# Kernel tuning notes

Measured on AMD Instinct MI355X. Metric: run time of the kernel, lower is better.

## Reference

```python
import jax, jax.numpy as jnp
import numpy as np

T, B, F = 512, 256, 256
H1, H2, OUT = 128, 64, 5


def _gru_layer(x, w_ih, w_hh, b_ih, b_hh):
    """PyTorch-convention GRU over time-major x [T, B, F_in] -> [T, B, H].
    Gate order in weights: r, z, n. n = tanh(Wn x + bn_i + r * (Un h + bn_h))."""
    H = w_hh.shape[1]
    # Precompute input projections for all timesteps: [T, B, 3H]
    xp = jnp.einsum('tbf,gf->tbg', x, w_ih) + b_ih

    def step(h, xp_t):
        hp = h @ w_hh.T + b_hh  # [B, 3H]
        xr, xz, xn = jnp.split(xp_t, 3, axis=-1)
        hr, hz, hn = jnp.split(hp, 3, axis=-1)
        r = jax.nn.sigmoid(xr + hr)
        z = jax.nn.sigmoid(xz + hz)
        n = jnp.tanh(xn + r * hn)
        h_new = (1.0 - z) * n + z * h
        return h_new, h_new

    h0 = jnp.zeros((x.shape[1], H), dtype=x.dtype)
    _, ys = jax.lax.scan(step, h0, xp)
    return ys  # [T, B, H]


def setup_inputs() -> dict:
    key = jax.random.key(0)
    ks = jax.random.split(key, 12)
    s1 = 1.0 / np.sqrt(H1)
    s2 = 1.0 / np.sqrt(H2)
    return {
        'x': jax.random.normal(ks[0], (T, B, F), dtype=jnp.float32),
        'w_ih1': jax.random.uniform(ks[1], (3 * H1, F), jnp.float32, -s1, s1),
        'w_hh1': jax.random.uniform(ks[2], (3 * H1, H1), jnp.float32, -s1, s1),
        'b_ih1': jax.random.uniform(ks[3], (3 * H1,), jnp.float32, -s1, s1),
        'b_hh1': jax.random.uniform(ks[4], (3 * H1,), jnp.float32, -s1, s1),
        'w_ih2': jax.random.uniform(ks[5], (3 * H2, H1), jnp.float32, -s2, s2),
        'w_hh2': jax.random.uniform(ks[6], (3 * H2, H2), jnp.float32, -s2, s2),
        'b_ih2': jax.random.uniform(ks[7], (3 * H2,), jnp.float32, -s2, s2),
        'b_hh2': jax.random.uniform(ks[8], (3 * H2,), jnp.float32, -s2, s2),
        'lin_w': jax.random.uniform(ks[9], (OUT, H2), jnp.float32, -s2, s2),
        'lin_b': jax.random.uniform(ks[10], (OUT,), jnp.float32, -s2, s2),
    }


def reference(x, w_ih1, w_hh1, b_ih1, b_hh1, w_ih2, w_hh2, b_ih2, b_hh2, lin_w, lin_b):
    h1 = _gru_layer(x, w_ih1, w_hh1, b_ih1, b_hh1)   # [T, B, 128]
    h2 = _gru_layer(h1, w_ih2, w_hh2, b_ih2, b_hh2)  # [T, B, 64]
    # Faithful to the original: x[:, -1, :] selects the last BATCH element
    # across all timesteps (time-major layout), giving [T, 64].
    last = h2[:, -1, :]
    return last @ lin_w.T + lin_b  # [T, 5]
```

## Files before the change

### kernel.cpp

```cpp
#include <hip/hip_runtime.h>
#include <hip/hip_bf16.h>

#define T_STEPS 512
#define BATCH   256
#define FDIM    256
#define H1      128
#define H2      64
#define OUT_N   5
#define CHUNK   8
#define NCHUNK  (T_STEPS / CHUNK)
#define LOG2E   1.4426950408889634f

#if __has_builtin(__builtin_amdgcn_exp2f)
#define EXP2F(x) __builtin_amdgcn_exp2f(x)
#else
#define EXP2F(x) exp2f(x)
#endif
#if __has_builtin(__builtin_amdgcn_rcpf)
#define RCPF(x) __builtin_amdgcn_rcpf(x)
#else
#define RCPF(x) (1.0f / (x))
#endif

template<int CTRL>
__device__ __forceinline__ float dpp_add(float v) {
    int s = __builtin_amdgcn_update_dpp(0, __float_as_int(v), CTRL, 0xF, 0xF, true);
    return v + __int_as_float(s);
}
__device__ __forceinline__ float sig_scaled(float a) {
    return RCPF(1.0f + EXP2F(a));
}
__device__ __forceinline__ float tanh_scaled(float a) {
    return fmaf(-2.0f, RCPF(EXP2F(a) + 1.0f), 1.0f);
}

__global__ __launch_bounds__(256) void xp1_kernel(
    const float* __restrict__ x,
    const float* __restrict__ w_ih1,
    const float* __restrict__ b_ih1,
    const float* __restrict__ b_hh1,
    float* __restrict__ xp)
{
    __shared__ float xrow[FDIM];
    const int t = blockIdx.x;
    const float* xr = x + (size_t)t * BATCH * FDIM + (size_t)(BATCH - 1) * FDIM;
    if (threadIdx.x < FDIM / 4) {
        ((float4*)xrow)[threadIdx.x] = ((const float4*)xr)[threadIdx.x];
    }
    __syncthreads();
    const int q = threadIdx.x >> 2;
    const int s = threadIdx.x & 3;
    #pragma unroll
    for (int pass = 0; pass < 6; ++pass) {
        const int g = pass * 64 + q;
        const float* w = w_ih1 + (size_t)g * FDIM + (s << 2);
        float acc = 0.0f;
        #pragma unroll
        for (int c = 0; c < 16; ++c) {
            float4 wv = *(const float4*)(w + 16 * c);
            const float* xv = xrow + (s << 2) + 16 * c;
            acc = fmaf(wv.x, xv[0], acc);
            acc = fmaf(wv.y, xv[1], acc);
            acc = fmaf(wv.z, xv[2], acc);
            acc = fmaf(wv.w, xv[3], acc);
        }
        acc = dpp_add<0xB1>(acc);
        acc = dpp_add<0x4E>(acc);
        if (s == 0) {
            const bool isN = (g >= 2 * H1);
            const float badd  = isN ? 0.0f : b_hh1[g];
            const float scale = isN ? (2.0f * LOG2E) : (-LOG2E);
            xp[t * (3 * H1) + g] = scale * (acc + b_ih1[g] + badd);
        }
    }
}

__global__ __launch_bounds__(512) void gru_pipe_kernel(
    const float* __restrict__ xp,
    const float* __restrict__ w_hh1, const float* __restrict__ b_hh1,
    const float* __restrict__ w_ih2, const float* __restrict__ b_ih2,
    const float* __restrict__ w_hh2, const float* __restrict__ b_hh2,
    float* __restrict__ g_h1, unsigned int* __restrict__ flags,
    float* __restrict__ h2_all)
{
    __shared__ float h1d[2][H1];
    __shared__ float h1chunk[CHUNK * H1];
    __shared__ float h2d[2][H2];
    const int tid = threadIdx.x;
    const float sRZ = -LOG2E, sN = 2.0f * LOG2E;

    if (blockIdx.x == 0) {
        const int g  = tid >> 3;
        const int s  = tid & 7;
        const int hi = (tid >> 2) & 1;
        const int r0 = 2 * g;

        float wr0[16], wz0[16], wn0[16], wr1[16], wz1[16], wn1[16];
        {
            const float* br0 = w_hh1 + (size_t)(         r0) * H1;
            const float* bz0 = w_hh1 + (size_t)(H1     + r0) * H1;
            const float* bn0 = w_hh1 + (size_t)(2 * H1 + r0) * H1;
            #pragma unroll
            for (int c = 0; c < 4; c++) {
                const int kk = (s << 2) + 32 * c;
                float4 v0 = *(const float4*)(br0 + kk);
                float4 v1 = *(const float4*)(bz0 + kk);
                float4 v2 = *(const float4*)(bn0 + kk);
                float4 v3 = *(const float4*)(br0 + H1 + kk);
                float4 v4 = *(const float4*)(bz0 + H1 + kk);
                float4 v5 = *(const float4*)(bn0 + H1 + kk);
                wr0[4*c+0]=sRZ*v0.x; wr0[4*c+1]=sRZ*v0.y; wr0[4*c+2]=sRZ*v0.z; wr0[4*c+3]=sRZ*v0.w;
                wz0[4*c+0]=sRZ*v1.x; wz0[4*c+1]=sRZ*v1.y; wz0[4*c+2]=sRZ*v1.z; wz0[4*c+3]=sRZ*v1.w;
                wn0[4*c+0]=sN *v2.x; wn0[4*c+1]=sN *v2.y; wn0[4*c+2]=sN *v2.z; wn0[4*c+3]=sN *v2.w;
                wr1[4*c+0]=sRZ*v3.x; wr1[4*c+1]=sRZ*v3.y; wr1[4*c+2]=sRZ*v3.z; wr1[4*c+3]=sRZ*v3.w;
                wz1[4*c+0]=sRZ*v4.x; wz1[4*c+1]=sRZ*v4.y; wz1[4*c+2]=sRZ*v4.z; wz1[4*c+3]=sRZ*v4.w;
                wn1[4*c+0]=sN *v5.x; wn1[4*c+1]=sN *v5.y; wn1[4*c+2]=sN *v5.z; wn1[4*c+3]=sN *v5.w;
            }
        }
        const float bn_a = sN * b_hh1[2 * H1 + r0];
        const float bn_b = sN * b_hh1[2 * H1 + r0 + 1];
        const float bh1n_s = hi ? bn_b : bn_a;

        if (tid < H1) { h1d[0][tid] = 0.0f; h1d[1][tid] = 0.0f; }
        float h1prev = 0.0f;
        float cxr, cxz, cxn;
        {
            float2 a2 = *(const float2*)(xp + r0);
            float2 b2 = *(const float2*)(xp + H1 + r0);
            float2 c2 = *(const float2*)(xp + 2 * H1 + r0);
            cxr = hi ? a2.y : a2.x; cxz = hi ? b2.y : b2.x; cxn = hi ? c2.y : c2.x;
        }
        __syncthreads();

        #pragma unroll 2
        for (int k = 0; k < T_STEPS; ++k) {
            const float* RP = h1d[(k + 1) & 1];
            float*       WP = h1d[k & 1];
            const float* hp = RP + (s << 2);
            float ar0=0.f, az0=0.f, an0=0.f, ar1=0.f, az1=0.f, an1=0.f;
            #pragma unroll
            for (int c = 0; c < 4; c++) {
                float4 h4 = *(const float4*)(hp + 32 * c);
                ar0=fmaf(wr0[4*c+0],h4.x,ar0); az0=fmaf(wz0[4*c+0],h4.x,az0); an0=fmaf(wn0[4*c+0],h4.x,an0);
                ar1=fmaf(wr1[4*c+0],h4.x,ar1); az1=fmaf(wz1[4*c+0],h4.x,az1); an1=fmaf(wn1[4*c+0],h4.x,an1);
                ar0=fmaf(wr0[4*c+1],h4.y,ar0); az0=fmaf(wz0[4*c+1],h4.y,az0); an0=fmaf(wn0[4*c+1],h4.y,an0);
                ar1=fmaf(wr1[4*c+1],h4.y,ar1); az1=fmaf(wz1[4*c+1],h4.y,az1); an1=fmaf(wn1[4*c+1],h4.y,an1);
                ar0=fmaf(wr0[4*c+2],h4.z,ar0); az0=fmaf(wz0[4*c+2],h4.z,az0); an0=fmaf(wn0[4*c+2],h4.z,an0);
                ar1=fmaf(wr1[4*c+2],h4.z,ar1); az1=fmaf(wz1[4*c+2],h4.z,az1); an1=fmaf(wn1[4*c+2],h4.z,an1);
                ar0=fmaf(wr0[4*c+3],h4.w,ar0); az0=fmaf(wz0[4*c+3],h4.w,az0); an0=fmaf(wn0[4*c+3],h4.w,an0);
                ar1=fmaf(wr1[4*c+3],h4.w,ar1); az1=fmaf(wz1[4*c+3],h4.w,az1); an1=fmaf(wn1[4*c+3],h4.w,an1);
            }
            float2 a2, b2, c2;
            {
                const int kn = (k < T_STEPS - 1) ? (k + 1) : (T_STEPS - 1);
                const float* nx = xp + (size_t)kn * (3 * H1);
                a2 = *(const float2*)(nx + r0);
                b2 = *(const float2*)(nx + H1 + r0);
                c2 = *(const float2*)(nx + 2 * H1 + r0);
            }
            ar0=dpp_add<0xB1>(ar0); ar0=dpp_add<0x4E>(ar0); ar0=dpp_add<0x141>(ar0);
            az0=dpp_add<0xB1>(az0); az0=dpp_add<0x4E>(az0); az0=dpp_add<0x141>(az0);
            an0=dpp_add<0xB1>(an0); an0=dpp_add<0x4E>(an0); an0=dpp_add<0x141>(an0);
            ar1=dpp_add<0xB1>(ar1); ar1=dpp_add<0x4E>(ar1); ar1=dpp_add<0x141>(ar1);
            az1=dpp_add<0xB1>(az1); az1=dpp_add<0x4E>(az1); az1=dpp_add<0x141>(az1);
            an1=dpp_add<0xB1>(an1); an1=dpp_add<0x4E>(an1); an1=dpp_add<0x141>(an1);
            const float ar = hi ? ar1 : ar0;
            const float az = hi ? az1 : az0;
            const float an = hi ? an1 : an0;
            const float r1g = sig_scaled(cxr + ar);
            const float z1g = sig_scaled(cxz + az);
            const float n1g = tanh_scaled(fmaf(r1g, an + bh1n_s, cxn));
            const float h1new = fmaf(z1g, h1prev - n1g, n1g);
            h1prev = h1new;
            if ((tid & 3) == 0) {
                WP[r0 + hi] = h1new;
                __hip_atomic_store((unsigned int*)g_h1 + (size_t)k * H1 + r0 + hi,
                                   __float_as_uint(h1new),
                                   __ATOMIC_RELAXED, __HIP_MEMORY_SCOPE_AGENT);
            }
            cxr = hi ? a2.y : a2.x; cxz = hi ? b2.y : b2.x; cxn = hi ? c2.y : c2.x;
            __syncthreads();
            if (((k & (CHUNK - 1)) == CHUNK - 1) && tid == 0) {
                __hip_atomic_store(&flags[k >> 3], 1u,
                                   __ATOMIC_RELEASE, __HIP_MEMORY_SCOPE_AGENT);
            }
        }
    } else {
        const int j2 = tid >> 3, s2 = tid & 7;
        float w2r[24], w2z[24], w2n[24];
        {
            const float* ir  = w_ih2 + (size_t)(         j2) * H1;
            const float* iz  = w_ih2 + (size_t)(H2     + j2) * H1;
            const float* inn = w_ih2 + (size_t)(2 * H2 + j2) * H1;
            #pragma unroll
            for (int c = 0; c < 4; c++) {
                const int kk = (s2 << 2) + 32 * c;
                float4 vr = *(const float4*)(ir  + kk);
                float4 vz = *(const float4*)(iz  + kk);
                float4 vn = *(const float4*)(inn + kk);
                w2r[4*c+0]=sRZ*vr.x; w2r[4*c+1]=sRZ*vr.y; w2r[4*c+2]=sRZ*vr.z; w2r[4*c+3]=sRZ*vr.w;
                w2z[4*c+0]=sRZ*vz.x; w2z[4*c+1]=sRZ*vz.y; w2z[4*c+2]=sRZ*vz.z; w2z[4*c+3]=sRZ*vz.w;
                w2n[4*c+0]=sN *vn.x; w2n[4*c+1]=sN *vn.y; w2n[4*c+2]=sN *vn.z; w2n[4*c+3]=sN *vn.w;
            }
            const float* hr = w_hh2 + (size_t)(         j2) * H2;
            const float* hz = w_hh2 + (size_t)(H2     + j2) * H2;
            const float* hn = w_hh2 + (size_t)(2 * H2 + j2) * H2;
            #pragma unroll
            for (int c = 0; c < 2; c++) {
                const int kk = (s2 << 2) + 32 * c;
                const int o = 4 * (c + 4);
                float4 vr = *(const float4*)(hr + kk);
                float4 vz = *(const float4*)(hz + kk);
                float4 vn = *(const float4*)(hn + kk);
                w2r[o+0]=sRZ*vr.x; w2r[o+1]=sRZ*vr.y; w2r[o+2]=sRZ*vr.z; w2r[o+3]=sRZ*vr.w;
                w2z[o+0]=sRZ*vz.x; w2z[o+1]=sRZ*vz.y; w2z[o+2]=sRZ*vz.z; w2z[o+3]=sRZ*vz.w;
                w2n[o+0]=sN *vn.x; w2n[o+1]=sN *vn.y; w2n[o+2]=sN *vn.z; w2n[o+3]=sN *vn.w;
            }
        }
        const float b2r_s  = sRZ * (b_ih2[j2]      + b_hh2[j2]);
        const float b2z_s  = sRZ * (b_ih2[H2 + j2] + b_hh2[H2 + j2]);
        const float b2xn_s = sN  *  b_ih2[2 * H2 + j2];
        const float b2hn_s = sN  *  b_hh2[2 * H2 + j2];
        float h2prev = 0.0f;
        if (tid < H2) { h2d[0][tid] = 0.0f; h2d[1][tid] = 0.0f; }
        __syncthreads();

        #pragma unroll 1
        for (int c = 0; c < NCHUNK; ++c) {
            while (__hip_atomic_load(&flags[c], __ATOMIC_ACQUIRE,
                                     __HIP_MEMORY_SCOPE_AGENT) != 1u) {
                __builtin_amdgcn_s_sleep(8);
            }
            unsigned long long v = __hip_atomic_load(
                (const unsigned long long*)g_h1 + (size_t)c * 512 + tid,
                __ATOMIC_RELAXED, __HIP_MEMORY_SCOPE_AGENT);
            ((unsigned long long*)h1chunk)[tid] = v;
            __syncthreads();

            #pragma unroll
            for (int i = 0; i < CHUNK; ++i) {
                const int t = c * CHUNK + i;
                const float* g1p = h1chunk + i * H1 + (s2 << 2);
                const float* g2p = h2d[(i + 1) & 1] + (s2 << 2);
                float a2r = 0.f, a2z = 0.f, axn = 0.f, ahn = 0.f;
                #pragma unroll
                for (int cc = 0; cc < 4; cc++) {
                    float4 g4 = *(const float4*)(g1p + 32 * cc);
                    a2r=fmaf(w2r[4*cc+0],g4.x,a2r); a2z=fmaf(w2z[4*cc+0],g4.x,a2z); axn=fmaf(w2n[4*cc+0],g4.x,axn);
                    a2r=fmaf(w2r[4*cc+1],g4.y,a2r); a2z=fmaf(w2z[4*cc+1],g4.y,a2z); axn=fmaf(w2n[4*cc+1],g4.y,axn);
                    a2r=fmaf(w2r[4*cc+2],g4.z,a2r); a2z=fmaf(w2z[4*cc+2],g4.z,a2z); axn=fmaf(w2n[4*cc+2],g4.z,axn);
                    a2r=fmaf(w2r[4*cc+3],g4.w,a2r); a2z=fmaf(w2z[4*cc+3],g4.w,a2z); axn=fmaf(w2n[4*cc+3],g4.w,axn);
                }
                #pragma unroll
                for (int cc = 4; cc < 6; cc++) {
                    float4 g4 = *(const float4*)(g2p + 32 * (cc - 4));
                    a2r=fmaf(w2r[4*cc+0],g4.x,a2r); a2z=fmaf(w2z[4*cc+0],g4.x,a2z); ahn=fmaf(w2n[4*cc+0],g4.x,ahn);
                    a2r=fmaf(w2r[4*cc+1],g4.y,a2r); a2z=fmaf(w2z[4*cc+1],g4.y,a2z); ahn=fmaf(w2n[4*cc+1],g4.y,ahn);
                    a2r=fmaf(w2r[4*cc+2],g4.z,a2r); a2z=fmaf(w2z[4*cc+2],g4.z,a2z); ahn=fmaf(w2n[4*cc+2],g4.z,ahn);
                    a2r=fmaf(w2r[4*cc+3],g4.w,a2r); a2z=fmaf(w2z[4*cc+3],g4.w,a2z); ahn=fmaf(w2n[4*cc+3],g4.w,ahn);
                }
                a2r=dpp_add<0xB1>(a2r); a2r=dpp_add<0x4E>(a2r); a2r=dpp_add<0x141>(a2r);
                a2z=dpp_add<0xB1>(a2z); a2z=dpp_add<0x4E>(a2z); a2z=dpp_add<0x141>(a2z);
                axn=dpp_add<0xB1>(axn); axn=dpp_add<0x4E>(axn); axn=dpp_add<0x141>(axn);
                ahn=dpp_add<0xB1>(ahn); ahn=dpp_add<0x4E>(ahn); ahn=dpp_add<0x141>(ahn);
                const float r2 = sig_scaled(a2r + b2r_s);
                const float z2 = sig_scaled(a2z + b2z_s);
                const float n2 = tanh_scaled(fmaf(r2, ahn + b2hn_s, axn + b2xn_s));
                const float h2new = fmaf(z2, h2prev - n2, n2);
                h2prev = h2new;
                if (s2 == 0) {
                    h2d[i & 1][j2] = h2new;
                    h2_all[(size_t)t * H2 + j2] = h2new;
                }
                __syncthreads();
            }
        }
    }
}

__global__ __launch_bounds__(256) void head_kernel(
    const float* __restrict__ h2_all,
    const float* __restrict__ lin_w,
    const float* __restrict__ lin_b,
    float* __restrict__ out)
{
    const int t = blockIdx.x * blockDim.x + threadIdx.x;
    if (t >= T_STEPS) return;
    const float* h = h2_all + t * H2;
    #pragma unroll
    for (int o = 0; o < OUT_N; o++) {
        float acc = lin_b[o];
        const float* w = lin_w + o * H2;
        #pragma unroll
        for (int j = 0; j < H2; j += 4) {
            float4 wv = *(const float4*)(w + j);
            float4 hv = *(const float4*)(h + j);
            acc = fmaf(wv.x, hv.x, acc);
            acc = fmaf(wv.y, hv.y, acc);
            acc = fmaf(wv.z, hv.z, acc);
            acc = fmaf(wv.w, hv.w, acc);
        }
        out[t * OUT_N + o] = acc;
    }
}

extern "C" void kernel_launch(void* const* d_in, const int* in_sizes, int n_in,
                              void* d_out, int out_size, void* d_ws, size_t ws_size,
                              hipStream_t stream) {
    const float* x     = (const float*)d_in[0];
    const float* w_ih1 = (const float*)d_in[1];
    const float* w_hh1 = (const float*)d_in[2];
    const float* b_ih1 = (const float*)d_in[3];
    const float* b_hh1 = (const float*)d_in[4];
    const float* w_ih2 = (const float*)d_in[5];
    const float* w_hh2 = (const float*)d_in[6];
    const float* b_ih2 = (const float*)d_in[7];
    const float* b_hh2 = (const float*)d_in[8];
    const float* lin_w = (const float*)d_in[9];
    const float* lin_b = (const float*)d_in[10];
    float* out = (float*)d_out;

    float* xp        = (float*)d_ws;
    float* h2_all    = xp + T_STEPS * 3 * H1;
    float* g_h1      = h2_all + T_STEPS * H2;
    unsigned int* fl = (unsigned int*)(g_h1 + T_STEPS * H1);

    hipMemsetAsync(fl, 0, NCHUNK * sizeof(unsigned int), stream);
    xp1_kernel<<<T_STEPS, 256, 0, stream>>>(x, w_ih1, b_ih1, b_hh1, xp);
    gru_pipe_kernel<<<2, 512, 0, stream>>>(xp, w_hh1, b_hh1,
                                           w_ih2, b_ih2, w_hh2, b_hh2,
                                           g_h1, fl, h2_all);
    head_kernel<<<(T_STEPS + 255) / 256, 256, 0, stream>>>(h2_all, lin_w, lin_b, out);
}
```

Baseline: 586.3 us.

## Use lightweight LDS-only barriers and chunk-unroll the layer-1 recurrence loop

Replaces __syncthreads with a custom barrier that waits only on LDS counters (lgkmcnt), so the per-step barrier no longer waits for outstanding global stores or loads such as the atomic h1 publish and the xp prefetch. Global memory counters are drained only once per chunk, just before the release flag is set. The layer-1 loop is restructured into chunk and inner-step loops with the inner loop fully unrolled, and the consumer's spin-sleep is shortened. The risk is ordering correctness: the memory model is being hand-managed, and the flag publish now depends on the explicit vmcnt wait.

```diff
diff --git a/kernel.cpp b/kernel.cpp
--- a/kernel.cpp
+++ b/kernel.cpp
@@ -21,6 +21,17 @@
 #else
 #define RCPF(x) (1.0f / (x))
 #endif
+
+#define BAR() do {                                              \
+    asm volatile("s_waitcnt lgkmcnt(0)" ::: "memory");          \
+    __builtin_amdgcn_s_barrier();                               \
+    __builtin_amdgcn_sched_barrier(0);                          \
+} while (0)
+#define VBAR() do {                                             \
+    asm volatile("s_waitcnt vmcnt(0) lgkmcnt(0)" ::: "memory"); \
+    __builtin_amdgcn_s_barrier();                               \
+    __builtin_amdgcn_sched_barrier(0);                          \
+} while (0)
 
 template<int CTRL>
 __device__ __forceinline__ float dpp_add(float v) {
@@ -130,59 +141,67 @@
             float2 c2 = *(const float2*)(xp + 2 * H1 + r0);
             cxr = hi ? a2.y : a2.x; cxz = hi ? b2.y : b2.x; cxn = hi ? c2.y : c2.x;
         }
-        __syncthreads();
-
-        #pragma unroll 2
-        for (int k = 0; k < T_STEPS; ++k) {
-            const float* RP = h1d[(k + 1) & 1];
-            float*       WP = h1d[k & 1];
-            const float* hp = RP + (s << 2);
-            float ar0=0.f, az0=0.f, an0=0.f, ar1=0.f, az1=0.f, an1=0.f;
-            #pragma unroll
-            for (int c = 0; c < 4; c++) {
-                float4 h4 = *(const float4*)(hp + 32 * c);
-                ar0=fmaf(wr0[4*c+0],h4.x,ar0); az0=fmaf(wz0[4*c+0],h4.x,az0); an0=fmaf(wn0[4*c+0],h4.x,an0);
-                ar1=fmaf(wr1[4*c+0],h4.x,ar1); az1=fmaf(wz1[4*c+0],h4.x,az1); an1=fmaf(wn1[4*c+0],h4.x,an1);
-                ar0=fmaf(wr0[4*c+1],h4.y,ar0); az0=fmaf(wz0[4*c+1],h4.y,az0); an0=fmaf(wn0[4*c+1],h4.y,an0);
-                ar1=fmaf(wr1[4*c+1],h4.y,ar1); az1=fmaf(wz1[4*c+1],h4.y,az1); an1=fmaf(wn1[4*c+1],h4.y,an1);
-                ar0=fmaf(wr0[4*c+2],h4.z,ar0); az0=fmaf(wz0[4*c+2],h4.z,az0); an0=fmaf(wn0[4*c+2],h4.z,an0);
-                ar1=fmaf(wr1[4*c+2],h4.z,ar1); az1=fmaf(wz1[4*c+2],h4.z,az1); an1=fmaf(wn1[4*c+2],h4.z,an1);
-                ar0=fmaf(wr0[4*c+3],h4.w,ar0); az0=fmaf(wz0[4*c+3],h4.w,az0); an0=fmaf(wn0[4*c+3],h4.w,an0);
-                ar1=fmaf(wr1[4*c+3],h4.w,ar1); az1=fmaf(wz1[4*c+3],h4.w,az1); an1=fmaf(wn1[4*c+3],h4.w,an1);
-            }
-            float2 a2, b2, c2;
-            {
-                const int kn = (k < T_STEPS - 1) ? (k + 1) : (T_STEPS - 1);
-                const float* nx = xp + (size_t)kn * (3 * H1);
-                a2 = *(const float2*)(nx + r0);
-                b2 = *(const float2*)(nx + H1 + r0);
-                c2 = *(const float2*)(nx + 2 * H1 + r0);
-            }
-            ar0=dpp_add<0xB1>(ar0); ar0=dpp_add<0x4E>(ar0); ar0=dpp_add<0x141>(ar0);
-            az0=dpp_add<0xB1>(az0); az0=dpp_add<0x4E>(az0); az0=dpp_add<0x141>(az0);
-            an0=dpp_add<0xB1>(an0); an0=dpp_add<0x4E>(an0); an0=dpp_add<0x141>(an0);
-            ar1=dpp_add<0xB1>(ar1); ar1=dpp_add<0x4E>(ar1); ar1=dpp_add<0x141>(ar1);
-            az1=dpp_add<0xB1>(az1); az1=dpp_add<0x4E>(az1); az1=dpp_add<0x141>(az1);
-            an1=dpp_add<0xB1>(an1); an1=dpp_add<0x4E>(an1); an1=dpp_add<0x141>(an1);
-            const float ar = hi ? ar1 : ar0;
-            const float az = hi ? az1 : az0;
-            const float an = hi ? an1 : an0;
-            const float r1g = sig_scaled(cxr + ar);
-            const float z1g = sig_scaled(cxz + az);
-            const float n1g = tanh_scaled(fmaf(r1g, an + bh1n_s, cxn));
-            const float h1new = fmaf(z1g, h1prev - n1g, n1g);
-            h1prev = h1new;
-            if ((tid & 3) == 0) {
-                WP[r0 + hi] = h1new;
-                __hip_atomic_store((unsigned int*)g_h1 + (size_t)k * H1 + r0 + hi,
-                                   __float_as_uint(h1new),
-                                   __ATOMIC_RELAXED, __HIP_MEMORY_SCOPE_AGENT);
-            }
-            cxr = hi ? a2.y : a2.x; cxz = hi ? b2.y : b2.x; cxn = hi ? c2.y : c2.x;
-            __syncthreads();
-            if (((k & (CHUNK - 1)) == CHUNK - 1) && tid == 0) {
-                __hip_atomic_store(&flags[k >> 3], 1u,
-                                   __ATOMIC_RELEASE, __HIP_MEMORY_SCOPE_AGENT);
+        BAR();
+
+        #pragma unroll 1
+        for (int c = 0; c < NCHUNK; ++c) {
+            #pragma unroll
+            for (int i = 0; i < CHUNK; ++i) {
+                const int k = c * CHUNK + i;
+                const float* RP = h1d[(i + 1) & 1];
+                float*       WP = h1d[i & 1];
+                const float* hp = RP + (s << 2);
+                float ar0=0.f, az0=0.f, an0=0.f, ar1=0.f, az1=0.f, an1=0.f;
+                #pragma unroll
+                for (int cc = 0; cc < 4; cc++) {
+                    float4 h4 = *(const float4*)(hp + 32 * cc);
+                    ar0=fmaf(wr0[4*cc+0],h4.x,ar0); az0=fmaf(wz0[4*cc+0],h4.x,az0); an0=fmaf(wn0[4*cc+0],h4.x,an0);
+                    ar1=fmaf(wr1[4*cc+0],h4.x,ar1); az1=fmaf(wz1[4*cc+0],h4.x,az1); an1=fmaf(wn1[4*cc+0],h4.x,an1);
+                    ar0=fmaf(wr0[4*cc+1],h4.y,ar0); az0=fmaf(wz0[4*cc+1],h4.y,az0); an0=fmaf(wn0[4*cc+1],h4.y,an0);
+                    ar1=fmaf(wr1[4*cc+1],h4.y,ar1); az1=fmaf(wz1[4*cc+1],h4.y,az1); an1=fmaf(wn1[4*cc+1],h4.y,an1);
+                    ar0=fmaf(wr0[4*cc+2],h4.z,ar0); az0=fmaf(wz0[4*cc+2],h4.z,az0); an0=fmaf(wn0[4*cc+2],h4.z,an0);
+                    ar1=fmaf(wr1[4*cc+2],h4.z,ar1); az1=fmaf(wz1[4*cc+2],h4.z,az1); an1=fmaf(wn1[4*cc+2],h4.z,an1);
+                    ar0=fmaf(wr0[4*cc+3],h4.w,ar0); az0=fmaf(wz0[4*cc+3],h4.w,az0); an0=fmaf(wn0[4*cc+3],h4.w,an0);
+                    ar1=fmaf(wr1[4*cc+3],h4.w,ar1); az1=fmaf(wz1[4*cc+3],h4.w,az1); an1=fmaf(wn1[4*cc+3],h4.w,an1);
+                }
+                float2 a2, b2, c2;
+                {
+                    const int kn = (k < T_STEPS - 1) ? (k + 1) : (T_STEPS - 1);
+                    const float* nx = xp + (size_t)kn * (3 * H1);
+                    a2 = *(const float2*)(nx + r0);
+                    b2 = *(const float2*)(nx + H1 + r0);
+                    c2 = *(const float2*)(nx + 2 * H1 + r0);
+                }
+                ar0=dpp_add<0xB1>(ar0); ar0=dpp_add<0x4E>(ar0); ar0=dpp_add<0x141>(ar0);
+                az0=dpp_add<0xB1>(az0); az0=dpp_add<0x4E>(az0); az0=dpp_add<0x141>(az0);
+                an0=dpp_add<0xB1>(an0); an0=dpp_add<0x4E>(an0); an0=dpp_add<0x141>(an0);
+                ar1=dpp_add<0xB1>(ar1); ar1=dpp_add<0x4E>(ar1); ar1=dpp_add<0x141>(ar1);
+                az1=dpp_add<0xB1>(az1); az1=dpp_add<0x4E>(az1); az1=dpp_add<0x141>(az1);
+                an1=dpp_add<0xB1>(an1); an1=dpp_add<0x4E>(an1); an1=dpp_add<0x141>(an1);
+                const float ar = hi ? ar1 : ar0;
+                const float az = hi ? az1 : az0;
+                const float an = hi ? an1 : an0;
+                const float r1g = sig_scaled(cxr + ar);
+                const float z1g = sig_scaled(cxz + az);
+                const float n1g = tanh_scaled(fmaf(r1g, an + bh1n_s, cxn));
+                const float h1new = fmaf(z1g, h1prev - n1g, n1g);
+                h1prev = h1new;
+                if ((tid & 3) == 0) {
+                    WP[r0 + hi] = h1new;
+                    __hip_atomic_store((unsigned int*)g_h1 + (size_t)k * H1 + r0 + hi,
+                                       __float_as_uint(h1new),
+                                       __ATOMIC_RELAXED, __HIP_MEMORY_SCOPE_AGENT);
+                }
+                cxr = hi ? a2.y : a2.x; cxz = hi ? b2.y : b2.x; cxn = hi ? c2.y : c2.x;
+                if (i == CHUNK - 1) {
+                    VBAR();
+                    if (tid == 0) {
+                        __hip_atomic_store(&flags[c], 1u,
+                                           __ATOMIC_RELEASE, __HIP_MEMORY_SCOPE_AGENT);
+                    }
+                } else {
+                    BAR();
+                }
             }
         }
     } else {
@@ -223,19 +242,19 @@
         const float b2hn_s = sN  *  b_hh2[2 * H2 + j2];
         float h2prev = 0.0f;
         if (tid < H2) { h2d[0][tid] = 0.0f; h2d[1][tid] = 0.0f; }
-        __syncthreads();
+        BAR();
 
         #pragma unroll 1
         for (int c = 0; c < NCHUNK; ++c) {
             while (__hip_atomic_load(&flags[c], __ATOMIC_ACQUIRE,
                                      __HIP_MEMORY_SCOPE_AGENT) != 1u) {
-                __builtin_amdgcn_s_sleep(8);
+                __builtin_amdgcn_s_sleep(1);
             }
             unsigned long long v = __hip_atomic_load(
                 (const unsigned long long*)g_h1 + (size_t)c * 512 + tid,
                 __ATOMIC_RELAXED, __HIP_MEMORY_SCOPE_AGENT);
             ((unsigned long long*)h1chunk)[tid] = v;
-            __syncthreads();
+            BAR();
 
             #pragma unroll
             for (int i = 0; i < CHUNK; ++i) {
@@ -272,7 +291,7 @@
                     h2d[i & 1][j2] = h2new;
                     h2_all[(size_t)t * H2 + j2] = h2new;
                 }
-                __syncthreads();
+                BAR();
             }
         }
     }
```

Measured after the change: 610.9 us. +4.2%, slower.
